# Performance work log

Measured on AMD Instinct MI355X. Metric: run time of the kernel, lower is better.

Reference implementation:

```python
import jax, jax.numpy as jnp
import numpy as np

B, N, D, H, C = 1, 256, 128, 4, 32
EPS = 1e-5

def setup_inputs() -> dict:
    key = jax.random.key(0)
    ks = jax.random.split(key, 10)
    s = 1.0 / np.sqrt(D)
    return {
        "Z_raw": jax.random.normal(ks[0], (B, N, N, D), dtype=jnp.float32),
        "Z_mask": jnp.ones((B, N, N), dtype=jnp.float32),
        "ln_w": jnp.ones((D,), dtype=jnp.float32),
        "ln_b": jnp.zeros((D,), dtype=jnp.float32),
        "b_proj_w": (jax.random.normal(ks[1], (H, D), dtype=jnp.float32) * s),
        "wq": jax.random.normal(ks[2], (D, H * C), dtype=jnp.float32) * s,
        "wk": jax.random.normal(ks[3], (D, H * C), dtype=jnp.float32) * s,
        "wv": jax.random.normal(ks[4], (D, H * C), dtype=jnp.float32) * s,
        "wg": jax.random.normal(ks[5], (D, H * C), dtype=jnp.float32) * s,
        "bg": jnp.ones((H * C,), dtype=jnp.float32),  # FastFold inits gating bias to 1
        "wo": jax.random.normal(ks[6], (H * C, D), dtype=jnp.float32) / np.sqrt(H * C),
        "out_bias": jnp.zeros((D,), dtype=jnp.float32),
    }

def reference(Z_raw, Z_mask, ln_w, ln_b, b_proj_w, wq, wk, wv, wg, bg, wo, out_bias):
    # LayerNorm over d_pair
    mu = jnp.mean(Z_raw, axis=-1, keepdims=True)
    var = jnp.mean(jnp.square(Z_raw - mu), axis=-1, keepdims=True)
    Z = (Z_raw - mu) * jax.lax.rsqrt(var + EPS) * ln_w + ln_b  # [B,N,N,D]

    # Triangle bias: b[b,h,q,k] (shared across rows i)
    tb = jnp.einsum('bqkd,hd->bhqk', Z, b_proj_w)  # [B,H,N,N]

    scale = 1.0 / np.sqrt(C)
    q = jnp.einsum('bijd,de->bije', Z, wq).reshape(B, N, N, H, C) * scale
    k = jnp.einsum('bijd,de->bije', Z, wk).reshape(B, N, N, H, C)
    v = jnp.einsum('bijd,de->bije', Z, wv).reshape(B, N, N, H, C)

    logits = jnp.einsum('biqhc,bikhc->bihqk', q, k)  # [B,I,H,N,N]
    mask_bias = 1e9 * (Z_mask - 1.0)  # [B,I,J]
    logits = logits + mask_bias[:, :, None, None, :] + tb[:, None]
    attn = jax.nn.softmax(logits, axis=-1)

    o = jnp.einsum('bihqk,bikhc->biqhc', attn, v)  # [B,I,N,H,C]
    gate = jax.nn.sigmoid(jnp.einsum('bijd,de->bije', Z, wg) + bg)
    o = o.reshape(B, N, N, H * C) * gate
    out = jnp.einsum('bije,ed->bijd', o, wo)

    # bias_dropout_add (eval mode: dropout is identity; dropout_mask is ones)
    return Z_raw + out + out_bias
```

## Files before the change

kernel.cpp:

```cpp
#include <hip/hip_runtime.h>
#include <hip/hip_bf16.h>


#define NN 256
#define DD 128
#define NP (NN*NN)

typedef __hip_bfloat16 bf16;
typedef unsigned short u16;
typedef unsigned int u32;
typedef __bf16 bf16x8 __attribute__((ext_vector_type(8)));
typedef float f32x4 __attribute__((ext_vector_type(4)));

__device__ __forceinline__ float b2f(bf16 x) { return __bfloat162float(x); }
__device__ __forceinline__ bf16 f2b(float x) { return __float2bfloat16(x); }
__device__ __forceinline__ float lo16(u32 u) { return __uint_as_float(u << 16); }
__device__ __forceinline__ float hi16(u32 u) { return __uint_as_float(u & 0xFFFF0000u); }
__device__ __forceinline__ float fexp2(float x) { return __builtin_amdgcn_exp2f(x); }
__device__ __forceinline__ bool bf16_mode(const void* lnw_raw) {
    return ((const u32*)lnw_raw)[0] == 0x3F803F80u;
}
__device__ __forceinline__ u32 pk2(float a, float b) {
    union { bf16 h; u16 u; } ca, cb; ca.h = f2b(a); cb.h = f2b(b);
    return ((u32)cb.u << 16) | (u32)ca.u;
}
__device__ __forceinline__ bf16x8 ld_frag(const u32* p) {
    uint4 r = *(const uint4*)p;
    return __builtin_bit_cast(bf16x8, r);
}
#define MFMA16(a,b,c) __builtin_amdgcn_mfma_f32_16x16x32_bf16(a,b,c,0,0,0)
#define LGKM0() asm volatile("s_waitcnt lgkmcnt(0)" ::: "memory")
#define PLANE(et) (((size_t)(et)) << 19)

#define OFF_ZM    0
#define OFF_LNW   65536
#define OFF_LNB   65664
#define OFF_BPW   65792
#define OFF_WQ    66304
#define OFF_WK    82688
#define OFF_WV    99072
#define OFF_WG    115456
#define OFF_BG    131840
#define OFF_WO    131968
#define OFF_OBIAS 148352
#define CANON_TOTAL 148480
#define OFF_WQT   148480
#define OFF_WKT   164864
#define OFF_WVT   181248
#define OFF_WGT   197632
#define OFF_WOT   214016
#define CANONT_TOTAL 81920

#define SCALE 0.17677669529663687f
#define LOG2E 1.4426950408889634f

__global__ __launch_bounds__(256) void k_conv(
    const void* zm, const void* lnw, const void* lnb, const void* bpw,
    const void* wq, const void* wk, const void* wv, const void* wg,
    const void* bg, const void* wo, const void* obias, bf16* canon)
{
    const bool bfm = bf16_mode(lnw);
    int idx = blockIdx.x * 256 + threadIdx.x;
    if (idx >= CANON_TOTAL) return;
    const void* src; int off;
    if      (idx < OFF_LNW)   { src = zm;    off = idx; }
    else if (idx < OFF_LNB)   { src = lnw;   off = idx - OFF_LNW; }
    else if (idx < OFF_BPW)   { src = lnb;   off = idx - OFF_LNB; }
    else if (idx < OFF_WQ)    { src = bpw;   off = idx - OFF_BPW; }
    else if (idx < OFF_WK)    { src = wq;    off = idx - OFF_WQ; }
    else if (idx < OFF_WV)    { src = wk;    off = idx - OFF_WK; }
    else if (idx < OFF_WG)    { src = wv;    off = idx - OFF_WV; }
    else if (idx < OFF_BG)    { src = wg;    off = idx - OFF_WG; }
    else if (idx < OFF_WO)    { src = bg;    off = idx - OFF_BG; }
    else if (idx < OFF_OBIAS) { src = wo;    off = idx - OFF_WO; }
    else                      { src = obias; off = idx - OFF_OBIAS; }
    float f = bfm ? b2f(((const bf16*)src)[off]) : ((const float*)src)[off];
    if (idx >= OFF_BPW && idx < OFF_WQ) f *= LOG2E;
    if (idx >= OFF_BG  && idx < OFF_WO) f *= LOG2E;
    canon[idx] = f2b(f);
}

__global__ __launch_bounds__(256) void k_convT(bf16* canon)
{
    int idx = blockIdx.x * 256 + threadIdx.x;
    if (idx >= CANONT_TOTAL) return;
    int m = idx >> 14, r = idx & 16383;
    int a = r >> 7, b = r & 127;
    int src = (m==0) ? OFF_WQ : (m==1) ? OFF_WK : (m==2) ? OFF_WV
            : (m==3) ? OFF_WG : OFF_WO;
    float v = b2f(canon[src + b*128 + a]);
    if (m == 0) v *= SCALE*LOG2E;
    if (m == 3) v *= LOG2E;
    canon[OFF_WQT + idx] = f2b(v);
}

__global__ __launch_bounds__(256, 3) void k_ln_qkv(
    const void* __restrict__ Zr, const void* __restrict__ lnw_raw,
    const bf16* __restrict__ canon,
    u32* __restrict__ znw, u32* __restrict__ qbw, u32* __restrict__ kbw,
    u32* __restrict__ vbTw, float* __restrict__ tbw)
{
    __shared__ u32 zs[64*68];
    const bool bfm = bf16_mode(lnw_raw);
    const u32* cw = (const u32*)canon;
    const int t = threadIdx.x;
    const int base = blockIdx.x * 64;
    const int p = t >> 2, l = t & 3;
    const int pair = base + p;

    float vals[32];
    if (bfm) {
        const u32* zr = (const u32*)Zr + (size_t)pair*64 + l*16;
        #pragma unroll
        for (int j = 0; j < 16; ++j) {
            u32 u = zr[j];
            vals[2*j] = lo16(u); vals[2*j+1] = hi16(u);
        }
    } else {
        const float* zr = (const float*)Zr + (size_t)pair*128 + l*32;
        #pragma unroll
        for (int j = 0; j < 32; ++j) vals[j] = zr[j];
    }

    float s = 0.f;
    #pragma unroll
    for (int m = 0; m < 32; ++m) s += vals[m];
    s += __shfl_xor(s, 1); s += __shfl_xor(s, 2);
    const float mu = s * (1.f/128.f);
    float s2 = 0.f;
    #pragma unroll
    for (int m = 0; m < 32; ++m) { float d = vals[m] - mu; s2 += d*d; }
    s2 += __shfl_xor(s2, 1); s2 += __shfl_xor(s2, 2);
    const float rstd = rsqrtf(s2 * (1.f/128.f) + 1e-5f);

    const u32* lnw_w = cw + (OFF_LNW>>1) + l*16;
    const u32* lnb_w = cw + (OFF_LNB>>1) + l*16;
    #pragma unroll
    for (int j = 0; j < 16; ++j) {
        u32 uw = lnw_w[j], ub = lnb_w[j];
        float z0 = (vals[2*j]  -mu)*rstd*lo16(uw) + lo16(ub);
        float z1 = (vals[2*j+1]-mu)*rstd*hi16(uw) + hi16(ub);
        zs[p*68 + l*16 + j] = pk2(z0, z1);
    }
    __syncthreads();

    #pragma unroll
    for (int j = 0; j < 16; ++j) {
        int idx = j*256 + t;
        znw[(size_t)base*64 + idx] = zs[(idx>>6)*68 + (idx&63)];
    }

    const int wv_ = t >> 6, lane = t & 63, qn = lane & 15, quad = lane >> 4;

    {
        f32x4 dtb = {0.f,0.f,0.f,0.f};
        #pragma unroll
        for (int ks = 0; ks < 4; ++ks) {
            bf16x8 a = ld_frag(cw + (OFF_BPW>>1) + qn*64 + ks*16 + quad*4);
            bf16x8 zbq = ld_frag(&zs[(wv_*16+qn)*68 + ks*16 + quad*4]);
            dtb = MFMA16(a, zbq, dtb);
        }
        if (quad == 0) {
            const int pc = base + wv_*16 + qn;
            tbw[0*NP + pc] = dtb[0];
            tbw[1*NP + pc] = dtb[1];
            tbw[2*NP + pc] = dtb[2];
            tbw[3*NP + pc] = dtb[3];
        }
    }

    const int ib = base >> 8;
    const int jbase = (base & 255);

    #pragma unroll
    for (int ei = 0; ei < 2; ++ei) {
        const int et = wv_*2 + ei;
        bf16x8 aq[4], ak[4], av[4];
        #pragma unroll
        for (int ks = 0; ks < 4; ++ks) {
            aq[ks] = ld_frag(cw + (OFF_WQT>>1) + (et*16+qn)*64 + ks*16 + quad*4);
            ak[ks] = ld_frag(cw + (OFF_WKT>>1) + (et*16+qn)*64 + ks*16 + quad*4);
            av[ks] = ld_frag(cw + (OFF_WVT>>1) + (et*16+qn)*64 + ks*16 + quad*4);
        }
        const int e = et*16 + qn;
        u32* vrow = vbTw + (size_t)((ib*4 + (e>>5))*32 + (e&31))*128;
        #pragma unroll
        for (int pg = 0; pg < 4; ++pg) {
            bf16x8 zb[4];
            #pragma unroll
            for (int ks = 0; ks < 4; ++ks)
                zb[ks] = ld_frag(&zs[(pg*16+qn)*68 + ks*16 + quad*4]);
            f32x4 dq = {0.f,0.f,0.f,0.f}, dk = {0.f,0.f,0.f,0.f}, dv = {0.f,0.f,0.f,0.f};
            #pragma unroll
            for (int ks = 0; ks < 4; ++ks) {
                dq = MFMA16(aq[ks], zb[ks], dq);
                dk = MFMA16(ak[ks], zb[ks], dk);
                dv = MFMA16(zb[ks], av[ks], dv);
            }
            const size_t pr = (size_t)(base + pg*16 + qn)*8 + quad*2;
            uint2 sq; sq.x = pk2(dq[0], dq[1]); sq.y = pk2(dq[2], dq[3]);
            *(uint2*)(qbw + PLANE(et) + pr) = sq;
            uint2 sk; sk.x = pk2(dk[0], dk[1]); sk.y = pk2(dk[2], dk[3]);
            *(uint2*)(kbw + PLANE(et) + pr) = sk;
            const int jj = jbase + pg*16 + quad*4;
            uint2 sv2; sv2.x = pk2(dv[0], dv[1]); sv2.y = pk2(dv[2], dv[3]);
            *(uint2*)(vrow + (jj>>1)) = sv2;
        }
    }
}

__global__ __launch_bounds__(256, 3) void k_attn(
    const u32* __restrict__ qb, const u32* __restrict__ kb,
    const u32* __restrict__ vbT, const bf16* __restrict__ canon,
    const float* __restrict__ tbw, u32* __restrict__ ob)
{
    __shared__ u32 ks_s[256*16];
    __shared__ u32 vs_s[32*132];
    __shared__ u32 p_s[4][16*68];
    const int t = threadIdx.x;
    const int i = blockIdx.x & 255, h = blockIdx.x >> 8;

    {
        const uint4* kp0 = (const uint4*)(kb + PLANE(2*h)   + (size_t)i*2048);
        const uint4* kp1 = (const uint4*)(kb + PLANE(2*h+1) + (size_t)i*2048);
        #pragma unroll
        for (int r = 0; r < 2; ++r) {
            int q4 = t + 256*r;
            int p = q4 >> 1;
            int c0 = (q4 & 1);
            int c1 = 2 + (q4 & 1);
            uint4 a = kp0[q4];
            *(uint4*)&ks_s[p*16 + ((c0 + (p>>1)) & 3)*4] = a;
            uint4 b = kp1[q4];
            *(uint4*)&ks_s[p*16 + ((c1 + (p>>1)) & 3)*4] = b;
        }
    }
    #pragma unroll
    for (int r = 0; r < 4; ++r) {
        int u = t + 256*r;
        int row = u >> 5, d4 = (u & 31)*4;
        *(uint4*)&vs_s[row*132 + d4] =
            *(const uint4*)(vbT + (size_t)((i*4+h)*32 + row)*128 + d4);
    }
    __syncthreads();

    const int wave = t >> 6, lane = t & 63;
    const int qn = lane & 15, quad = lane >> 4;
    u32* pw = p_s[wave];
    const int ksw = ((quad + (qn>>1)) & 3) * 4;

    f32x4 mb[16];
    #pragma unroll
    for (int kt = 0; kt < 16; ++kt) {
        uint2 zm2 = *(const uint2*)((const u32*)canon + (OFF_ZM>>1) + i*128 + kt*8 + quad*2);
        mb[kt][0] = 1.4426950e9f*(lo16(zm2.x)-1.f);
        mb[kt][1] = 1.4426950e9f*(hi16(zm2.x)-1.f);
        mb[kt][2] = 1.4426950e9f*(lo16(zm2.y)-1.f);
        mb[kt][3] = 1.4426950e9f*(hi16(zm2.y)-1.f);
    }

    for (int qt = 0; qt < 4; ++qt) {
        const int qg = wave*64 + qt*16 + qn;

        f32x4 sv[16];
        const float* tbq = tbw + h*NP + qg*256 + quad*4;
        #pragma unroll
        for (int kt = 0; kt < 16; ++kt)
            sv[kt] = *(const f32x4*)(tbq + kt*16) + mb[kt];

        bf16x8 qf = ld_frag(qb + PLANE(2*h + (quad>>1)) + (size_t)(i*256+qg)*8 + (quad&1)*4);
        #pragma unroll
        for (int kt = 0; kt < 16; ++kt) {
            bf16x8 kf = ld_frag(&ks_s[(kt*16+qn)*16 + ksw]);
            sv[kt] = MFMA16(kf, qf, sv[kt]);
        }

        float sum = 0.f;
        #pragma unroll
        for (int kt = 0; kt < 16; ++kt) {
            #pragma unroll
            for (int r = 0; r < 4; ++r) {
                float e = fexp2(sv[kt][r]);
                sv[kt][r] = e; sum += e;
            }
        }
        sum += __shfl_xor(sum, 16);
        sum += __shfl_xor(sum, 32);

        f32x4 o0 = {0.f,0.f,0.f,0.f}, o1 = {0.f,0.f,0.f,0.f};
        #pragma unroll
        for (int hf = 0; hf < 2; ++hf) {
            #pragma unroll
            for (int kt = 0; kt < 8; ++kt) {
                int kg = hf*8 + kt;
                uint2 w;
                w.x = pk2(sv[kg][0], sv[kg][1]);
                w.y = pk2(sv[kg][2], sv[kg][3]);
                *(uint2*)&pw[qn*68 + kt*8 + quad*2] = w;
            }
            LGKM0();
            #pragma unroll
            for (int ch = 0; ch < 4; ++ch) {
                bf16x8 pf = ld_frag(&pw[qn*68 + ch*16 + quad*4]);
                bf16x8 v0 = ld_frag(&vs_s[qn*132      + hf*64 + ch*16 + quad*4]);
                bf16x8 v1 = ld_frag(&vs_s[(16+qn)*132 + hf*64 + ch*16 + quad*4]);
                o0 = MFMA16(v0, pf, o0);
                o1 = MFMA16(v1, pf, o1);
            }
        }

        const float rinv = 1.f / sum;
        uint2 s0, s1;
        s0.x = pk2(o0[0]*rinv, o0[1]*rinv); s0.y = pk2(o0[2]*rinv, o0[3]*rinv);
        s1.x = pk2(o1[0]*rinv, o1[1]*rinv); s1.y = pk2(o1[2]*rinv, o1[3]*rinv);
        u32* opb = ob + PLANE(2*h) + (size_t)(i*256+qg)*8 + quad*2;
        *(uint2*)opb = s0;
        *(uint2*)(opb + (1u<<19)) = s1;
    }
}

__global__ __launch_bounds__(256, 3) void k_gateout(
    const void* __restrict__ Zr, const void* __restrict__ lnw_raw,
    const bf16* __restrict__ canon,
    const u32* __restrict__ znw, const u32* __restrict__ obw,
    void* __restrict__ outp)
{
    __shared__ u32 og_s[64*68];
    const bool bfm = bf16_mode(lnw_raw);
    const u32* cw = (const u32*)canon;
    const int t = threadIdx.x;
    const int base = blockIdx.x * 64;
    const int wv_ = t >> 6, lane = t & 63, qn = lane & 15, quad = lane >> 4;

    bf16x8 awg[2][4];
    uint2 bg2[2];
    #pragma unroll
    for (int ei = 0; ei < 2; ++ei) {
        const int et = wv_*2 + ei;
        #pragma unroll
        for (int ks = 0; ks < 4; ++ks)
            awg[ei][ks] = ld_frag(cw + (OFF_WGT>>1) + (et*16+qn)*64 + ks*16 + quad*4);
        bg2[ei] = *(const uint2*)(cw + (OFF_BG>>1) + et*8 + quad*2);
    }
    #pragma unroll
    for (int pg = 0; pg < 4; ++pg) {
        const size_t pair = base + pg*16 + qn;
        bf16x8 zb[4];
        #pragma unroll
        for (int ks = 0; ks < 4; ++ks)
            zb[ks] = ld_frag(znw + pair*64 + ks*16 + quad*4);
        #pragma unroll
        for (int ei = 0; ei < 2; ++ei) {
            const int et = wv_*2 + ei;
            f32x4 ag = {0.f,0.f,0.f,0.f};
            #pragma unroll
            for (int ks = 0; ks < 4; ++ks) ag = MFMA16(awg[ei][ks], zb[ks], ag);
            uint2 ob2 = *(const uint2*)(obw + PLANE(et) + pair*8 + quad*2);
            float r0 = lo16(ob2.x) / (1.f + fexp2(-(ag[0] + lo16(bg2[ei].x))));
            float r1 = hi16(ob2.x) / (1.f + fexp2(-(ag[1] + hi16(bg2[ei].x))));
            float r2 = lo16(ob2.y) / (1.f + fexp2(-(ag[2] + lo16(bg2[ei].y))));
            float r3 = hi16(ob2.y) / (1.f + fexp2(-(ag[3] + hi16(bg2[ei].y))));
            uint2 w; w.x = pk2(r0, r1); w.y = pk2(r2, r3);
            *(uint2*)&og_s[(pg*16+qn)*68 + et*8 + quad*2] = w;
        }
    }
    __syncthreads();

    bf16x8 awo[2][4];
    uint2 oi2[2];
    #pragma unroll
    for (int di = 0; di < 2; ++di) {
        const int dt = wv_*2 + di;
        #pragma unroll
        for (int ks = 0; ks < 4; ++ks)
            awo[di][ks] = ld_frag(cw + (OFF_WOT>>1) + (dt*16+qn)*64 + ks*16 + quad*4);
        oi2[di] = *(const uint2*)(cw + (OFF_OBIAS>>1) + dt*8 + quad*2);
    }
    #pragma unroll
    for (int pg = 0; pg < 4; ++pg) {
        const size_t pair = base + pg*16 + qn;
        const size_t prow = pair*64;
        bf16x8 ogb[4];
        #pragma unroll
        for (int ks = 0; ks < 4; ++ks)
            ogb[ks] = ld_frag(&og_s[(pg*16+qn)*68 + ks*16 + quad*4]);
        #pragma unroll
        for (int di = 0; di < 2; ++di) {
            const int dt = wv_*2 + di;
            f32x4 ao = {0.f,0.f,0.f,0.f};
            #pragma unroll
            for (int ks = 0; ks < 4; ++ks) ao = MFMA16(awo[di][ks], ogb[ks], ao);
            const float b0 = lo16(oi2[di].x), b1 = hi16(oi2[di].x);
            const float b2v = lo16(oi2[di].y), b3 = hi16(oi2[di].y);
            if (bfm) {
                uint2 zr2 = *(const uint2*)((const u32*)Zr + prow + dt*8 + quad*2);
                uint2 w;
                w.x = pk2(ao[0] + b0 + lo16(zr2.x), ao[1] + b1 + hi16(zr2.x));
                w.y = pk2(ao[2] + b2v + lo16(zr2.y), ao[3] + b3 + hi16(zr2.y));
                *(uint2*)((u32*)outp + prow + dt*8 + quad*2) = w;
            } else {
                const float* zr = (const float*)Zr + pair*128 + dt*16 + quad*4;
                float4 z4 = *(const float4*)zr;
                float4 w;
                w.x = ao[0] + b0 + z4.x;  w.y = ao[1] + b1 + z4.y;
                w.z = ao[2] + b2v + z4.z; w.w = ao[3] + b3 + z4.w;
                *(float4*)((float*)outp + pair*128 + dt*16 + quad*4) = w;
            }
        }
    }
}

extern "C" void kernel_launch(void* const* d_in, const int* in_sizes, int n_in,
                              void* d_out, int out_size, void* d_ws, size_t ws_size,
                              hipStream_t stream)
{
    const void* Zr    = d_in[0];
    const void* Zm    = d_in[1];
    const void* lnw   = d_in[2];
    const void* lnb   = d_in[3];
    const void* bpw   = d_in[4];
    const void* wq    = d_in[5];
    const void* wk    = d_in[6];
    const void* wv    = d_in[7];
    const void* wg    = d_in[8];
    const void* bg    = d_in[9];
    const void* wo    = d_in[10];
    const void* obias = d_in[11];

    char* ws = (char*)d_ws;
    const size_t M = 16777216;
    u32* znw   = (u32*)(ws);
    u32* qbw   = (u32*)(ws + 1*M);
    u32* kbw   = (u32*)(ws + 2*M);
    u32* vbTw  = (u32*)(ws + 3*M);
    u32* obw   = (u32*)(ws + 4*M);
    float* tbw = (float*)(ws + 5*M);
    bf16* canon = (bf16*)(ws + 5*M + 1048576);

    hipLaunchKernelGGL(k_conv, dim3((CANON_TOTAL+255)/256), dim3(256), 0, stream,
                       Zm, lnw, lnb, bpw, wq, wk, wv, wg, bg, wo, obias, canon);
    hipLaunchKernelGGL(k_convT, dim3((CANONT_TOTAL+255)/256), dim3(256), 0, stream,
                       canon);
    hipLaunchKernelGGL(k_ln_qkv, dim3(1024), dim3(256), 0, stream,
                       Zr, lnw, canon, znw, qbw, kbw, vbTw, tbw);
    hipLaunchKernelGGL(k_attn, dim3(1024), dim3(256), 0, stream,
                       qbw, kbw, vbTw, canon, tbw, obw);
    hipLaunchKernelGGL(k_gateout, dim3(1024), dim3(256), 0, stream,
                       Zr, lnw, canon, znw, obw, d_out);
}
```

Baseline: 203.6 us.

## Feed softmax probabilities straight from registers into K=16 MFMA for PV

The attention kernel no longer stages exponentiated probabilities through a per-wave shared-memory buffer. It packs them in registers and feeds them directly as operands of the 16x16x16 bf16 MFMA, whose accumulator layout matches the input fragment layout. V in LDS uses an XOR swizzle instead of padding, which frees shared memory, and launch bounds rise to 4 blocks per CU. This removes the LDS round-trip and wait, but it doubles the MFMA instruction count with the smaller-K variant.

```diff
diff --git a/kernel.cpp b/kernel.cpp
--- a/kernel.cpp
+++ b/kernel.cpp
@@ -10,6 +10,7 @@
 typedef unsigned short u16;
 typedef unsigned int u32;
 typedef __bf16 bf16x8 __attribute__((ext_vector_type(8)));
+typedef short s16x4 __attribute__((ext_vector_type(4)));
 typedef float f32x4 __attribute__((ext_vector_type(4)));
 
 __device__ __forceinline__ float b2f(bf16 x) { return __bfloat162float(x); }
@@ -29,7 +30,7 @@
     return __builtin_bit_cast(bf16x8, r);
 }
 #define MFMA16(a,b,c) __builtin_amdgcn_mfma_f32_16x16x32_bf16(a,b,c,0,0,0)
-#define LGKM0() asm volatile("s_waitcnt lgkmcnt(0)" ::: "memory")
+#define MFMA16K(a,b,c) __builtin_amdgcn_mfma_f32_16x16x16bf16_1k(a,b,c,0,0,0)
 #define PLANE(et) (((size_t)(et)) << 19)
 
 #define OFF_ZM    0
@@ -209,14 +210,13 @@
     }
 }
 
-__global__ __launch_bounds__(256, 3) void k_attn(
+__global__ __launch_bounds__(256, 4) void k_attn(
     const u32* __restrict__ qb, const u32* __restrict__ kb,
     const u32* __restrict__ vbT, const bf16* __restrict__ canon,
     const float* __restrict__ tbw, u32* __restrict__ ob)
 {
     __shared__ u32 ks_s[256*16];
-    __shared__ u32 vs_s[32*132];
-    __shared__ u32 p_s[4][16*68];
+    __shared__ u32 vs_s[32*128];
     const int t = threadIdx.x;
     const int i = blockIdx.x & 255, h = blockIdx.x >> 8;
 
@@ -239,15 +239,15 @@
     for (int r = 0; r < 4; ++r) {
         int u = t + 256*r;
         int row = u >> 5, d4 = (u & 31)*4;
-        *(uint4*)&vs_s[row*132 + d4] =
+        *(uint4*)&vs_s[row*128 + (d4 ^ ((row & 7) << 2))] =
             *(const uint4*)(vbT + (size_t)((i*4+h)*32 + row)*128 + d4);
     }
     __syncthreads();
 
     const int wave = t >> 6, lane = t & 63;
     const int qn = lane & 15, quad = lane >> 4;
-    u32* pw = p_s[wave];
     const int ksw = ((quad + (qn>>1)) & 3) * 4;
+    const int vswz = (qn & 7) << 2;
 
     f32x4 mb[16];
     #pragma unroll
@@ -276,38 +276,22 @@
         }
 
         float sum = 0.f;
+        f32x4 o0 = {0.f,0.f,0.f,0.f}, o1 = {0.f,0.f,0.f,0.f};
         #pragma unroll
         for (int kt = 0; kt < 16; ++kt) {
-            #pragma unroll
-            for (int r = 0; r < 4; ++r) {
-                float e = fexp2(sv[kt][r]);
-                sv[kt][r] = e; sum += e;
-            }
+            float e0 = fexp2(sv[kt][0]), e1 = fexp2(sv[kt][1]);
+            float e2 = fexp2(sv[kt][2]), e3 = fexp2(sv[kt][3]);
+            sum += (e0 + e1) + (e2 + e3);
+            uint2 pw2; pw2.x = pk2(e0, e1); pw2.y = pk2(e2, e3);
+            s16x4 pf = __builtin_bit_cast(s16x4, pw2);
+            const int vcol = (kt*8 + quad*2) ^ vswz;
+            s16x4 v0 = __builtin_bit_cast(s16x4, *(const uint2*)&vs_s[qn*128 + vcol]);
+            s16x4 v1 = __builtin_bit_cast(s16x4, *(const uint2*)&vs_s[(16+qn)*128 + vcol]);
+            o0 = MFMA16K(v0, pf, o0);
+            o1 = MFMA16K(v1, pf, o1);
         }
         sum += __shfl_xor(sum, 16);
         sum += __shfl_xor(sum, 32);
-
-        f32x4 o0 = {0.f,0.f,0.f,0.f}, o1 = {0.f,0.f,0.f,0.f};
-        #pragma unroll
-        for (int hf = 0; hf < 2; ++hf) {
-            #pragma unroll
-            for (int kt = 0; kt < 8; ++kt) {
-                int kg = hf*8 + kt;
-                uint2 w;
-                w.x = pk2(sv[kg][0], sv[kg][1]);
-                w.y = pk2(sv[kg][2], sv[kg][3]);
-                *(uint2*)&pw[qn*68 + kt*8 + quad*2] = w;
-            }
-            LGKM0();
-            #pragma unroll
-            for (int ch = 0; ch < 4; ++ch) {
-                bf16x8 pf = ld_frag(&pw[qn*68 + ch*16 + quad*4]);
-                bf16x8 v0 = ld_frag(&vs_s[qn*132      + hf*64 + ch*16 + quad*4]);
-                bf16x8 v1 = ld_frag(&vs_s[(16+qn)*132 + hf*64 + ch*16 + quad*4]);
-                o0 = MFMA16(v0, pf, o0);
-                o1 = MFMA16(v1, pf, o1);
-            }
-        }
 
         const float rinv = 1.f / sum;
         uint2 s0, s1;
```

Result: slower. 305.5 us (+50.1%).
